# Performance work log

Hardware: AMD Instinct MI355X
Metric: run time of the kernel (lower is better)

## Reference

```python
import jax, jax.numpy as jnp
import numpy as np
import math

B, H, S, D = 4, 16, 2048, 64

def setup_inputs() -> dict:
    key = jax.random.key(0)
    kq, kk, kv, km = jax.random.split(key, 4)
    query = jax.random.normal(kq, (B, H, S, D), dtype=jnp.float32)
    k = jax.random.normal(kk, (B, H, S, D), dtype=jnp.float32)
    value = jax.random.normal(kv, (B, H, S, D), dtype=jnp.float32)
    mask = jax.random.randint(km, (1, 1, S, S), 0, 2) == 1  # True = masked
    return {"query": query, "key": k, "value": value, "mask": mask}

def reference(query, key, value, mask):
    # scores: [B,H,S,S]
    scale = 1.0 / math.sqrt(key.shape[-1])
    scores = jnp.einsum('bhqd,bhkd->bhqk', query, key) * scale
    scores = jnp.where(mask, -jnp.inf, scores)
    probs = jax.nn.softmax(scores, axis=-1)
    out = jnp.einsum('bhqk,bhkd->bhqd', probs, value)
    return out
```

## Files before the change

### kernel.cpp

```cpp
#include <hip/hip_runtime.h>
#include <hip/hip_bf16.h>
#include <stdint.h>

#define BHN 64
#define SEQ 2048
#define DH  64

typedef unsigned short u16;
typedef __attribute__((ext_vector_type(8))) short bf16x8;
typedef __attribute__((ext_vector_type(16))) float f32x16;

__device__ inline u16 f2bf(float x){
  union { float f; uint32_t u; } a; a.f = x;
  uint32_t u = a.u;
  uint32_t lsb = (u >> 16) & 1u;
  u += 0x7FFFu + lsb;
  return (u16)(u >> 16);
}

__device__ inline float fast_exp2(float x){
#if __has_builtin(__builtin_amdgcn_exp2f)
  return __builtin_amdgcn_exp2f(x);
#else
  float r; asm("v_exp_f32 %0, %1" : "=v"(r) : "v"(x)); return r;
#endif
}

__device__ inline void gload_lds16(const void* g, void* l){
  __builtin_amdgcn_global_load_lds(
      (const __attribute__((address_space(1))) void*)g,
      (__attribute__((address_space(3))) void*)l, 16, 0, 0);
}


__global__ __launch_bounds__(256) void build_tiles(const float* __restrict__ kf,
                                                   const float* __restrict__ vf,
                                                   u16* __restrict__ tiles){
  __shared__ float sVf[64][65];
  int head = blockIdx.x >> 5;
  int kt   = blockIdx.x & 31;
  int k0   = kt * 64;
  int t = threadIdx.x;

  {
    int r = t >> 2;
    int dseg = (t & 3) * 16;
    const float* src = vf + ((int64_t)(head*SEQ + k0 + r))*DH + dseg;
    #pragma unroll
    for (int j = 0; j < 16; j += 4){
      float4 v = *(const float4*)(src + j);
      sVf[r][dseg+j+0] = v.x; sVf[r][dseg+j+1] = v.y;
      sVf[r][dseg+j+2] = v.z; sVf[r][dseg+j+3] = v.w;
    }
  }

  u16* outb = tiles + ((size_t)(head*32 + kt) << 13);

  #pragma unroll
  for (int i = 0; i < 2; i++){
    int cid = i*256 + t;
    int f = cid >> 6;
    int l = cid & 63;
    int kh = f >> 2, ds = f & 3;
    int row = k0 + kh*32 + (l & 31);
    int dstart = ds*16 + (l >> 5)*8;
    const float* src = kf + ((int64_t)(head*SEQ + row))*DH + dstart;
    float4 a = *(const float4*)(src);
    float4 b = *(const float4*)(src + 4);
    union { u16 h[8]; uint4 v; } pk;
    pk.h[0]=f2bf(a.x); pk.h[1]=f2bf(a.y); pk.h[2]=f2bf(a.z); pk.h[3]=f2bf(a.w);
    pk.h[4]=f2bf(b.x); pk.h[5]=f2bf(b.y); pk.h[6]=f2bf(b.z); pk.h[7]=f2bf(b.w);
    *(uint4*)(outb + f*512 + l*8) = pk.v;
  }

  __syncthreads();

  #pragma unroll
  for (int i = 0; i < 2; i++){
    int cid = i*256 + t;
    int g = cid >> 6;
    int l = cid & 63;
    int oh = g >> 2, ks = g & 3;
    int d  = oh*32 + (l & 31);
    int kk = ks*16 + (l >> 5)*8;
    union { u16 h[8]; uint4 v; } pk;
    #pragma unroll
    for (int j = 0; j < 8; j++) pk.h[j] = f2bf(sVf[kk+j][d]);
    *(uint4*)(outb + (8+g)*512 + l*8) = pk.v;
  }
}

__global__ __launch_bounds__(256) void pack_mask(const void* __restrict__ mraw,
                                                 uint32_t* __restrict__ mkp){
  __shared__ int sflag;
  int t = threadIdx.x;
  const uint32_t* m32 = (const uint32_t*)mraw;
  if (t == 0) sflag = 0;
  __syncthreads();
  if (t < 64){
    uint32_t v = m32[t] | m32[t+64] | m32[t+128] | m32[t+192];
    if (v > 1u) atomicOr(&sflag, 1);
  }
  __syncthreads();
  bool isbool = (sflag != 0);
  int idx = blockIdx.x*256 + t;
  int row = idx >> 6;
  int wd  = idx & 63;
  uint32_t bits = 0;
  if (isbool){
    const uint8_t* mb = (const uint8_t*)mraw + (int64_t)row*SEQ + wd*32;
    uint4 a = ((const uint4*)mb)[0];
    uint4 b = ((const uint4*)mb)[1];
    uint32_t words[8] = {a.x,a.y,a.z,a.w,b.x,b.y,b.z,b.w};
    #pragma unroll
    for (int i = 0; i < 32; i++){
      int kl = (i&3) + 8*((i>>2)&3) + 4*(i>>4);
      uint32_t byte = (words[kl>>2] >> (8*(kl&3))) & 0xFFu;
      bits |= (byte ? 0u : 1u) << i;
    }
  } else {
    const uint32_t* mi = m32 + (int64_t)row*SEQ + wd*32;
    uint32_t words[32];
    #pragma unroll
    for (int j = 0; j < 32; j += 4){
      uint4 v = *(const uint4*)(mi + j);
      words[j+0]=v.x; words[j+1]=v.y; words[j+2]=v.z; words[j+3]=v.w;
    }
    #pragma unroll
    for (int i = 0; i < 32; i++){
      int kl = (i&3) + 8*((i>>2)&3) + 4*(i>>4);
      bits |= (words[kl] ? 0u : 1u) << i;
    }
  }
  mkp[(size_t)wd*SEQ + row] = bits;
}


__global__ __launch_bounds__(256, 4) void attn_mfma(
    const float* __restrict__ qf, const u16* __restrict__ tiles,
    const uint32_t* __restrict__ mkp, float* __restrict__ out)
{
  __shared__ __align__(16) char lds[2*8192 + 512];

  int bid = blockIdx.x;
  int logical = (bid & 7)*128 + (bid >> 3);
  int head = logical >> 4;
  int q0   = (logical & 15) * 128;

  int t  = threadIdx.x;
  int w  = t >> 6;
  int l  = t & 63;
  int l31 = l & 31;
  int hi  = l >> 5;
  int hi16 = hi << 4;

  const float QS = 0.125f * 1.4426950408889634f;
  bf16x8 qfr[4];
  {
    const float* qrow = qf + ((size_t)(head*SEQ + q0 + w*32 + l31))*DH + hi*8;
    #pragma unroll
    for (int ds = 0; ds < 4; ds++){
      float4 a = *(const float4*)(qrow + ds*16);
      float4 b = *(const float4*)(qrow + ds*16 + 4);
      uint32_t u0, u1, u2, u3;
      asm("v_cvt_pk_bf16_f32 %0, %1, %2" : "=v"(u0) : "v"(a.x*QS), "v"(a.y*QS));
      asm("v_cvt_pk_bf16_f32 %0, %1, %2" : "=v"(u1) : "v"(a.z*QS), "v"(a.w*QS));
      asm("v_cvt_pk_bf16_f32 %0, %1, %2" : "=v"(u2) : "v"(b.x*QS), "v"(b.y*QS));
      asm("v_cvt_pk_bf16_f32 %0, %1, %2" : "=v"(u3) : "v"(b.z*QS), "v"(b.w*QS));
      union { uint32_t u[4]; bf16x8 h; } pk_;
      pk_.u[0]=u0; pk_.u[1]=u1; pk_.u[2]=u2; pk_.u[3]=u3;
      qfr[ds] = pk_.h;
    }
  }

  const uint32_t* mptr = mkp + (q0 + w*32 + l31);

  const char* tb = (const char*)tiles + ((size_t)head << 19) + l*16;
  int woff  = (w < 2) ? (w*2048) : (8192 + (w & 1)*4096);
  int khmul = (w < 2) ? 4096 : 2048;
  char* dbase = lds + w*2048;

  f32x16 O0 = {0,0,0,0,0,0,0,0,0,0,0,0,0,0,0,0};
  f32x16 O1 = {0,0,0,0,0,0,0,0,0,0,0,0,0,0,0,0};
  float ls0 = 0.f, ls1 = 0.f;

  const char* ldsL = lds + l*16;

  auto STAGE = [&](int ks32, int bufoff){
    int ktp = (ks32 < 64) ? ks32 : 63;
    const char* s_ = tb + (((size_t)(ktp >> 1)) << 14) + woff + (ktp & 1)*khmul;
    char* d_ = dbase + bufoff;
    gload_lds16(s_,        d_);
    gload_lds16(s_ + 1024, d_ + 1024);
  };

  STAGE(0, 0);
  __syncthreads();

  int cur = 0;
  for (int kt = 0; kt < 64; kt++){
    if (kt < 63) STAGE(kt+1, cur ^ 8192);
    uint32_t mw = *mptr; mptr += SEQ;
    uint32_t wsh = mw >> hi16;

    f32x16 c = {0,0,0,0,0,0,0,0,0,0,0,0,0,0,0,0};
    __builtin_amdgcn_s_setprio(1);
    #pragma unroll
    for (int ds = 0; ds < 4; ds++){
      bf16x8 kfr = *(const bf16x8*)(ldsL + cur + ds*1024);
      c = __builtin_amdgcn_mfma_f32_32x32x16_bf16(kfr, qfr[ds], c, 0, 0, 0);
    }
    __builtin_amdgcn_s_setprio(0);

    float p[16];
    #pragma unroll
    for (int r = 0; r < 16; r++){
      float pe = fast_exp2(c[r]);
      int32_t km;
      asm("v_bfe_i32 %0, %1, %2, 1" : "=v"(km) : "v"(wsh), "n"(r));
      p[r] = __uint_as_float(__float_as_uint(pe) & (uint32_t)km);
    }
    #pragma unroll
    for (int r = 0; r < 8; r++){ ls0 += p[r]; ls1 += p[r+8]; }

    bf16x8 pa0, pa1;
    {
      uint32_t A0, A1, B0, B1;
      asm("v_cvt_pk_bf16_f32 %0, %1, %2" : "=v"(A0) : "v"(p[0]), "v"(p[1]));
      asm("v_cvt_pk_bf16_f32 %0, %1, %2" : "=v"(A1) : "v"(p[2]), "v"(p[3]));
      asm("v_cvt_pk_bf16_f32 %0, %1, %2" : "=v"(B0) : "v"(p[4]), "v"(p[5]));
      asm("v_cvt_pk_bf16_f32 %0, %1, %2" : "=v"(B1) : "v"(p[6]), "v"(p[7]));
      asm("v_permlane32_swap_b32 %0, %1" : "+v"(A0), "+v"(B0));
      asm("v_permlane32_swap_b32 %0, %1" : "+v"(A1), "+v"(B1));
      union { uint32_t u[4]; bf16x8 h; } pk_;
      pk_.u[0] = A0; pk_.u[1] = A1; pk_.u[2] = B0; pk_.u[3] = B1;
      pa0 = pk_.h;
    }
    {
      uint32_t A0, A1, B0, B1;
      asm("v_cvt_pk_bf16_f32 %0, %1, %2" : "=v"(A0) : "v"(p[8]),  "v"(p[9]));
      asm("v_cvt_pk_bf16_f32 %0, %1, %2" : "=v"(A1) : "v"(p[10]), "v"(p[11]));
      asm("v_cvt_pk_bf16_f32 %0, %1, %2" : "=v"(B0) : "v"(p[12]), "v"(p[13]));
      asm("v_cvt_pk_bf16_f32 %0, %1, %2" : "=v"(B1) : "v"(p[14]), "v"(p[15]));
      asm("v_permlane32_swap_b32 %0, %1" : "+v"(A0), "+v"(B0));
      asm("v_permlane32_swap_b32 %0, %1" : "+v"(A1), "+v"(B1));
      union { uint32_t u[4]; bf16x8 h; } pk_;
      pk_.u[0] = A0; pk_.u[1] = A1; pk_.u[2] = B0; pk_.u[3] = B1;
      pa1 = pk_.h;
    }

    __builtin_amdgcn_s_setprio(1);
    {
      bf16x8 v00 = *(const bf16x8*)(ldsL + cur + 4096);
      bf16x8 v01 = *(const bf16x8*)(ldsL + cur + 5120);
      bf16x8 v10 = *(const bf16x8*)(ldsL + cur + 6144);
      bf16x8 v11 = *(const bf16x8*)(ldsL + cur + 7168);
      O0 = __builtin_amdgcn_mfma_f32_32x32x16_bf16(pa0, v00, O0, 0, 0, 0);
      O0 = __builtin_amdgcn_mfma_f32_32x32x16_bf16(pa1, v01, O0, 0, 0, 0);
      O1 = __builtin_amdgcn_mfma_f32_32x32x16_bf16(pa0, v10, O1, 0, 0, 0);
      O1 = __builtin_amdgcn_mfma_f32_32x32x16_bf16(pa1, v11, O1, 0, 0, 0);
    }
    __builtin_amdgcn_s_setprio(0);

    __syncthreads();
    cur ^= 8192;
  }

  float lt = ls0 + ls1;
  {
    uint32_t a = __float_as_uint(lt), b = a;
    asm("v_permlane32_swap_b32 %0, %1" : "+v"(a), "+v"(b));
    lt = __uint_as_float(a) + __uint_as_float(b);
  }
  float* sInv = (float*)(lds + 16384);
  if (hi == 0) sInv[w*32 + l31] = 1.0f / lt;
  float* obase = out + ((size_t)(head*SEQ + q0 + w*32))*DH + l31;
  #pragma unroll
  for (int r = 0; r < 16; r++){
    int qr = (r&3) + 8*(r>>2) + 4*hi;
    float inv = sInv[w*32 + qr];
    obase[(size_t)qr*DH]      = O0[r] * inv;
    obase[(size_t)qr*DH + 32] = O1[r] * inv;
  }
}


__global__ __launch_bounds__(256) void attn_naive(
    const float* __restrict__ qf, const float* __restrict__ kf,
    const float* __restrict__ vf, const void* __restrict__ mraw,
    float* __restrict__ out)
{
  __shared__ float sq[64];
  __shared__ float sS[SEQ];
  __shared__ float redM[4], redS[4];
  __shared__ float sO[4][64];
  __shared__ int sflag;

  int bid = blockIdx.x;
  int bh = bid >> 11;
  int q  = bid & 2047;
  int t  = threadIdx.x;
  const uint32_t* m32 = (const uint32_t*)mraw;
  if (t == 0) sflag = 0;
  __syncthreads();
  if (t < 64){
    uint32_t v = m32[t] | m32[t+64] | m32[t+128] | m32[t+192];
    if (v > 1u) atomicOr(&sflag, 1);
  }
  if (t < 64) sq[t] = qf[((int64_t)bh*SEQ + q)*DH + t] * (0.125f*1.4426950408889634f);
  __syncthreads();
  bool isbool = (sflag != 0);

  float lmax = -3e38f;
  for (int k = t; k < SEQ; k += 256){
    bool masked = isbool ? (((const uint8_t*)mraw)[(int64_t)q*SEQ + k] != 0)
                         : (m32[(int64_t)q*SEQ + k] != 0);
    float s = -3e38f;
    if (!masked){
      const float* krow = kf + ((int64_t)bh*SEQ + k)*DH;
      float acc = 0.f;
      for (int d = 0; d < 64; d++) acc += sq[d]*krow[d];
      s = acc;
    }
    sS[k] = s;
    lmax = fmaxf(lmax, s);
  }
  for (int o = 32; o >= 1; o >>= 1) lmax = fmaxf(lmax, __shfl_xor(lmax, o));
  if ((t & 63) == 0) redM[t >> 6] = lmax;
  __syncthreads();
  float m = fmaxf(fmaxf(redM[0], redM[1]), fmaxf(redM[2], redM[3]));
  float lsum = 0.f;
  for (int k = t; k < SEQ; k += 256){
    float p = exp2f(sS[k] - m);
    sS[k] = p;
    lsum += p;
  }
  for (int o = 32; o >= 1; o >>= 1) lsum += __shfl_xor(lsum, o);
  if ((t & 63) == 0) redS[t >> 6] = lsum;
  __syncthreads();
  float lden = redS[0] + redS[1] + redS[2] + redS[3];

  float o = 0.f;
  int d = t & 63;
  int c = t >> 6;
  for (int k = c*512; k < (c+1)*512; k++)
    o += sS[k] * vf[((int64_t)bh*SEQ + k)*DH + d];
  sO[c][d] = o;
  __syncthreads();
  if (t < 64){
    float r = (sO[0][t] + sO[1][t] + sO[2][t] + sO[3][t]) / lden;
    out[((int64_t)bh*SEQ + q)*DH + t] = r;
  }
}


extern "C" void kernel_launch(void* const* d_in, const int* in_sizes, int n_in,
                              void* d_out, int out_size, void* d_ws, size_t ws_size,
                              hipStream_t stream)
{
  const float* qf = (const float*)d_in[0];
  const float* kf = (const float*)d_in[1];
  const float* vf = (const float*)d_in[2];
  const void*  mraw = d_in[3];
  float* out = (float*)d_out;

  size_t tilesB = (size_t)BHN*32*16384;
  size_t need = tilesB + (size_t)SEQ*64*4 + 256;
  if (ws_size >= need){
    u16* tiles = (u16*)d_ws;
    uint32_t* mkp = (uint32_t*)((char*)d_ws + tilesB);
    hipLaunchKernelGGL(build_tiles, dim3(2048), dim3(256), 0, stream, kf, vf, tiles);
    hipLaunchKernelGGL(pack_mask,   dim3(512),  dim3(256), 0, stream, mraw, mkp);
    hipLaunchKernelGGL(attn_mfma,   dim3(1024), dim3(256), 0, stream, qf, tiles, mkp, out);
  } else {
    hipLaunchKernelGGL(attn_naive, dim3(BHN*SEQ), dim3(256), 0, stream, qf, kf, vf, mraw, out);
  }
}
```

Before: 118.8 us.

## Process 64-key tiles per barrier with interleaved 64-bit mask words

Result: faster. 112.3 us (-5.5%).

```diff
diff --git a/kernel.cpp b/kernel.cpp
--- a/kernel.cpp
+++ b/kernel.cpp
@@ -132,7 +132,7 @@
       bits |= (words[kl] ? 0u : 1u) << i;
     }
   }
-  mkp[(size_t)wd*SEQ + row] = bits;
+  mkp[((size_t)(wd >> 1)*SEQ + row)*2 + (wd & 1)] = bits;
 }
 
 
@@ -140,7 +140,7 @@
     const float* __restrict__ qf, const u16* __restrict__ tiles,
     const uint32_t* __restrict__ mkp, float* __restrict__ out)
 {
-  __shared__ __align__(16) char lds[2*8192 + 512];
+  __shared__ __align__(16) char lds[2*16384 + 512];
 
   int bid = blockIdx.x;
   int logical = (bid & 7)*128 + (bid >> 3);
@@ -173,12 +173,10 @@
     }
   }
 
-  const uint32_t* mptr = mkp + (q0 + w*32 + l31);
-
-  const char* tb = (const char*)tiles + ((size_t)head << 19) + l*16;
-  int woff  = (w < 2) ? (w*2048) : (8192 + (w & 1)*4096);
-  int khmul = (w < 2) ? 4096 : 2048;
-  char* dbase = lds + w*2048;
+  const uint2* mptr = (const uint2*)mkp + (q0 + w*32 + l31);
+
+  const char* tb = (const char*)tiles + ((size_t)head << 19) + w*4096 + l*16;
+  char* dwave = lds + w*4096;
 
   f32x16 O0 = {0,0,0,0,0,0,0,0,0,0,0,0,0,0,0,0};
   f32x16 O1 = {0,0,0,0,0,0,0,0,0,0,0,0,0,0,0,0};
@@ -186,84 +184,96 @@
 
   const char* ldsL = lds + l*16;
 
-  auto STAGE = [&](int ks32, int bufoff){
-    int ktp = (ks32 < 64) ? ks32 : 63;
-    const char* s_ = tb + (((size_t)(ktp >> 1)) << 14) + woff + (ktp & 1)*khmul;
-    char* d_ = dbase + bufoff;
+  auto STAGE = [&](int kt64, int bufoff){
+    const char* s_ = tb + ((size_t)kt64 << 14);
+    char* d_ = dwave + bufoff;
     gload_lds16(s_,        d_);
     gload_lds16(s_ + 1024, d_ + 1024);
+    gload_lds16(s_ + 2048, d_ + 2048);
+    gload_lds16(s_ + 3072, d_ + 3072);
   };
 
   STAGE(0, 0);
+  uint2 mw2 = *mptr; mptr += SEQ;
   __syncthreads();
 
   int cur = 0;
-  for (int kt = 0; kt < 64; kt++){
-    if (kt < 63) STAGE(kt+1, cur ^ 8192);
-    uint32_t mw = *mptr; mptr += SEQ;
-    uint32_t wsh = mw >> hi16;
-
-    f32x16 c = {0,0,0,0,0,0,0,0,0,0,0,0,0,0,0,0};
-    __builtin_amdgcn_s_setprio(1);
-    #pragma unroll
-    for (int ds = 0; ds < 4; ds++){
-      bf16x8 kfr = *(const bf16x8*)(ldsL + cur + ds*1024);
-      c = __builtin_amdgcn_mfma_f32_32x32x16_bf16(kfr, qfr[ds], c, 0, 0, 0);
-    }
-    __builtin_amdgcn_s_setprio(0);
-
-    float p[16];
-    #pragma unroll
-    for (int r = 0; r < 16; r++){
-      float pe = fast_exp2(c[r]);
-      int32_t km;
-      asm("v_bfe_i32 %0, %1, %2, 1" : "=v"(km) : "v"(wsh), "n"(r));
-      p[r] = __uint_as_float(__float_as_uint(pe) & (uint32_t)km);
-    }
-    #pragma unroll
-    for (int r = 0; r < 8; r++){ ls0 += p[r]; ls1 += p[r+8]; }
-
-    bf16x8 pa0, pa1;
-    {
-      uint32_t A0, A1, B0, B1;
-      asm("v_cvt_pk_bf16_f32 %0, %1, %2" : "=v"(A0) : "v"(p[0]), "v"(p[1]));
-      asm("v_cvt_pk_bf16_f32 %0, %1, %2" : "=v"(A1) : "v"(p[2]), "v"(p[3]));
-      asm("v_cvt_pk_bf16_f32 %0, %1, %2" : "=v"(B0) : "v"(p[4]), "v"(p[5]));
-      asm("v_cvt_pk_bf16_f32 %0, %1, %2" : "=v"(B1) : "v"(p[6]), "v"(p[7]));
-      asm("v_permlane32_swap_b32 %0, %1" : "+v"(A0), "+v"(B0));
-      asm("v_permlane32_swap_b32 %0, %1" : "+v"(A1), "+v"(B1));
-      union { uint32_t u[4]; bf16x8 h; } pk_;
-      pk_.u[0] = A0; pk_.u[1] = A1; pk_.u[2] = B0; pk_.u[3] = B1;
-      pa0 = pk_.h;
-    }
-    {
-      uint32_t A0, A1, B0, B1;
-      asm("v_cvt_pk_bf16_f32 %0, %1, %2" : "=v"(A0) : "v"(p[8]),  "v"(p[9]));
-      asm("v_cvt_pk_bf16_f32 %0, %1, %2" : "=v"(A1) : "v"(p[10]), "v"(p[11]));
-      asm("v_cvt_pk_bf16_f32 %0, %1, %2" : "=v"(B0) : "v"(p[12]), "v"(p[13]));
-      asm("v_cvt_pk_bf16_f32 %0, %1, %2" : "=v"(B1) : "v"(p[14]), "v"(p[15]));
-      asm("v_permlane32_swap_b32 %0, %1" : "+v"(A0), "+v"(B0));
-      asm("v_permlane32_swap_b32 %0, %1" : "+v"(A1), "+v"(B1));
-      union { uint32_t u[4]; bf16x8 h; } pk_;
-      pk_.u[0] = A0; pk_.u[1] = A1; pk_.u[2] = B0; pk_.u[3] = B1;
-      pa1 = pk_.h;
-    }
-
-    __builtin_amdgcn_s_setprio(1);
-    {
-      bf16x8 v00 = *(const bf16x8*)(ldsL + cur + 4096);
-      bf16x8 v01 = *(const bf16x8*)(ldsL + cur + 5120);
-      bf16x8 v10 = *(const bf16x8*)(ldsL + cur + 6144);
-      bf16x8 v11 = *(const bf16x8*)(ldsL + cur + 7168);
-      O0 = __builtin_amdgcn_mfma_f32_32x32x16_bf16(pa0, v00, O0, 0, 0, 0);
-      O0 = __builtin_amdgcn_mfma_f32_32x32x16_bf16(pa1, v01, O0, 0, 0, 0);
-      O1 = __builtin_amdgcn_mfma_f32_32x32x16_bf16(pa0, v10, O1, 0, 0, 0);
-      O1 = __builtin_amdgcn_mfma_f32_32x32x16_bf16(pa1, v11, O1, 0, 0, 0);
-    }
-    __builtin_amdgcn_s_setprio(0);
-
+  for (int kt = 0; kt < 32; kt++){
+    uint2 mw2n = mw2;
+    if (kt < 31){
+      STAGE(kt+1, cur ^ 16384);
+      mw2n = *mptr; mptr += SEQ;
+    }
+
+    const char* lb = ldsL + cur;
+
+    #pragma unroll
+    for (int g = 0; g < 2; g++){
+      uint32_t wsh = (g ? mw2.y : mw2.x) >> hi16;
+
+      f32x16 c = {0,0,0,0,0,0,0,0,0,0,0,0,0,0,0,0};
+      __builtin_amdgcn_s_setprio(1);
+      #pragma unroll
+      for (int ds = 0; ds < 4; ds++){
+        bf16x8 kfr = *(const bf16x8*)(lb + (4*g + ds)*1024);
+        c = __builtin_amdgcn_mfma_f32_32x32x16_bf16(kfr, qfr[ds], c, 0, 0, 0);
+      }
+      __builtin_amdgcn_s_setprio(0);
+
+      float p[16];
+      #pragma unroll
+      for (int r = 0; r < 16; r++){
+        float pe = fast_exp2(c[r]);
+        int32_t km;
+        asm("v_bfe_i32 %0, %1, %2, 1" : "=v"(km) : "v"(wsh), "n"(r));
+        p[r] = __uint_as_float(__float_as_uint(pe) & (uint32_t)km);
+      }
+      #pragma unroll
+      for (int r = 0; r < 8; r++){ ls0 += p[r]; ls1 += p[r+8]; }
+
+      bf16x8 pa0, pa1;
+      {
+        uint32_t A0, A1, B0, B1;
+        asm("v_cvt_pk_bf16_f32 %0, %1, %2" : "=v"(A0) : "v"(p[0]), "v"(p[1]));
+        asm("v_cvt_pk_bf16_f32 %0, %1, %2" : "=v"(A1) : "v"(p[2]), "v"(p[3]));
+        asm("v_cvt_pk_bf16_f32 %0, %1, %2" : "=v"(B0) : "v"(p[4]), "v"(p[5]));
+        asm("v_cvt_pk_bf16_f32 %0, %1, %2" : "=v"(B1) : "v"(p[6]), "v"(p[7]));
+        asm("v_permlane32_swap_b32 %0, %1" : "+v"(A0), "+v"(B0));
+        asm("v_permlane32_swap_b32 %0, %1" : "+v"(A1), "+v"(B1));
+        union { uint32_t u[4]; bf16x8 h; } pk_;
+        pk_.u[0] = A0; pk_.u[1] = A1; pk_.u[2] = B0; pk_.u[3] = B1;
+        pa0 = pk_.h;
+      }
+      {
+        uint32_t A0, A1, B0, B1;
+        asm("v_cvt_pk_bf16_f32 %0, %1, %2" : "=v"(A0) : "v"(p[8]),  "v"(p[9]));
+        asm("v_cvt_pk_bf16_f32 %0, %1, %2" : "=v"(A1) : "v"(p[10]), "v"(p[11]));
+        asm("v_cvt_pk_bf16_f32 %0, %1, %2" : "=v"(B0) : "v"(p[12]), "v"(p[13]));
+        asm("v_cvt_pk_bf16_f32 %0, %1, %2" : "=v"(B1) : "v"(p[14]), "v"(p[15]));
+        asm("v_permlane32_swap_b32 %0, %1" : "+v"(A0), "+v"(B0));
+        asm("v_permlane32_swap_b32 %0, %1" : "+v"(A1), "+v"(B1));
+        union { uint32_t u[4]; bf16x8 h; } pk_;
+        pk_.u[0] = A0; pk_.u[1] = A1; pk_.u[2] = B0; pk_.u[3] = B1;
+        pa1 = pk_.h;
+      }
+
+      __builtin_amdgcn_s_setprio(1);
+      {
+        bf16x8 v00 = *(const bf16x8*)(lb + (8  + 2*g)*1024);
+        bf16x8 v01 = *(const bf16x8*)(lb + (9  + 2*g)*1024);
+        bf16x8 v10 = *(const bf16x8*)(lb + (12 + 2*g)*1024);
+        bf16x8 v11 = *(const bf16x8*)(lb + (13 + 2*g)*1024);
+        O0 = __builtin_amdgcn_mfma_f32_32x32x16_bf16(pa0, v00, O0, 0, 0, 0);
+        O0 = __builtin_amdgcn_mfma_f32_32x32x16_bf16(pa1, v01, O0, 0, 0, 0);
+        O1 = __builtin_amdgcn_mfma_f32_32x32x16_bf16(pa0, v10, O1, 0, 0, 0);
+        O1 = __builtin_amdgcn_mfma_f32_32x32x16_bf16(pa1, v11, O1, 0, 0, 0);
+      }
+      __builtin_amdgcn_s_setprio(0);
+    }
+
+    mw2 = mw2n;
     __syncthreads();
-    cur ^= 8192;
+    cur ^= 16384;
   }
 
   float lt = ls0 + ls1;
@@ -272,7 +282,7 @@
     asm("v_permlane32_swap_b32 %0, %1" : "+v"(a), "+v"(b));
     lt = __uint_as_float(a) + __uint_as_float(b);
   }
-  float* sInv = (float*)(lds + 16384);
+  float* sInv = (float*)(lds + 32768);
   if (hi == 0) sInv[w*32 + l31] = 1.0f / lt;
   float* obase = out + ((size_t)(head*SEQ + q0 + w*32))*DH + l31;
   #pragma unroll
```

## Load K/V fragments directly from global into registers, dropping LDS staging

Applied to the files above, without the earlier changes.

Result: no change. 117.3 us (-1.3%).

```diff
diff --git a/kernel.cpp b/kernel.cpp
--- a/kernel.cpp
+++ b/kernel.cpp
@@ -24,12 +24,6 @@
 #else
   float r; asm("v_exp_f32 %0, %1" : "=v"(r) : "v"(x)); return r;
 #endif
-}
-
-__device__ inline void gload_lds16(const void* g, void* l){
-  __builtin_amdgcn_global_load_lds(
-      (const __attribute__((address_space(1))) void*)g,
-      (__attribute__((address_space(3))) void*)l, 16, 0, 0);
 }
 
 
@@ -132,15 +126,15 @@
       bits |= (words[kl] ? 0u : 1u) << i;
     }
   }
-  mkp[(size_t)wd*SEQ + row] = bits;
-}
-
-
-__global__ __launch_bounds__(256, 4) void attn_mfma(
+  mkp[((size_t)(wd >> 1)*SEQ + row)*2 + (wd & 1)] = bits;
+}
+
+
+__global__ __launch_bounds__(256, 3) void attn_mfma(
     const float* __restrict__ qf, const u16* __restrict__ tiles,
     const uint32_t* __restrict__ mkp, float* __restrict__ out)
 {
-  __shared__ __align__(16) char lds[2*8192 + 512];
+  __shared__ float sInv[128];
 
   int bid = blockIdx.x;
   int logical = (bid & 7)*128 + (bid >> 3);
@@ -173,43 +167,37 @@
     }
   }
 
-  const uint32_t* mptr = mkp + (q0 + w*32 + l31);
+  const uint2* mptr = (const uint2*)mkp + (q0 + w*32 + l31);
 
   const char* tb = (const char*)tiles + ((size_t)head << 19) + l*16;
-  int woff  = (w < 2) ? (w*2048) : (8192 + (w & 1)*4096);
-  int khmul = (w < 2) ? 4096 : 2048;
-  char* dbase = lds + w*2048;
 
   f32x16 O0 = {0,0,0,0,0,0,0,0,0,0,0,0,0,0,0,0};
   f32x16 O1 = {0,0,0,0,0,0,0,0,0,0,0,0,0,0,0,0};
   float ls0 = 0.f, ls1 = 0.f;
 
-  const char* ldsL = lds + l*16;
-
-  auto STAGE = [&](int ks32, int bufoff){
-    int ktp = (ks32 < 64) ? ks32 : 63;
-    const char* s_ = tb + (((size_t)(ktp >> 1)) << 14) + woff + (ktp & 1)*khmul;
-    char* d_ = dbase + bufoff;
-    gload_lds16(s_,        d_);
-    gload_lds16(s_ + 1024, d_ + 1024);
+  auto LOADK = [&](int sg, bf16x8* kb){
+    const char* s_ = tb + ((size_t)(sg >> 1) << 14) + (sg & 1)*4096;
+    kb[0] = *(const bf16x8*)(s_);
+    kb[1] = *(const bf16x8*)(s_ + 1024);
+    kb[2] = *(const bf16x8*)(s_ + 2048);
+    kb[3] = *(const bf16x8*)(s_ + 3072);
   };
-
-  STAGE(0, 0);
-  __syncthreads();
-
-  int cur = 0;
-  for (int kt = 0; kt < 64; kt++){
-    if (kt < 63) STAGE(kt+1, cur ^ 8192);
-    uint32_t mw = *mptr; mptr += SEQ;
-    uint32_t wsh = mw >> hi16;
+  auto LOADV = [&](int sg, bf16x8* vb){
+    const char* s_ = tb + ((size_t)(sg >> 1) << 14) + 8192 + (sg & 1)*2048;
+    vb[0] = *(const bf16x8*)(s_);
+    vb[1] = *(const bf16x8*)(s_ + 1024);
+    vb[2] = *(const bf16x8*)(s_ + 4096);
+    vb[3] = *(const bf16x8*)(s_ + 5120);
+  };
+
+  auto COMPUTE = [&](const bf16x8* kb, const bf16x8* vb, uint32_t mword){
+    uint32_t wsh = mword >> hi16;
 
     f32x16 c = {0,0,0,0,0,0,0,0,0,0,0,0,0,0,0,0};
     __builtin_amdgcn_s_setprio(1);
     #pragma unroll
-    for (int ds = 0; ds < 4; ds++){
-      bf16x8 kfr = *(const bf16x8*)(ldsL + cur + ds*1024);
-      c = __builtin_amdgcn_mfma_f32_32x32x16_bf16(kfr, qfr[ds], c, 0, 0, 0);
-    }
+    for (int ds = 0; ds < 4; ds++)
+      c = __builtin_amdgcn_mfma_f32_32x32x16_bf16(kb[ds], qfr[ds], c, 0, 0, 0);
     __builtin_amdgcn_s_setprio(0);
 
     float p[16];
@@ -250,20 +238,31 @@
     }
 
     __builtin_amdgcn_s_setprio(1);
-    {
-      bf16x8 v00 = *(const bf16x8*)(ldsL + cur + 4096);
-      bf16x8 v01 = *(const bf16x8*)(ldsL + cur + 5120);
-      bf16x8 v10 = *(const bf16x8*)(ldsL + cur + 6144);
-      bf16x8 v11 = *(const bf16x8*)(ldsL + cur + 7168);
-      O0 = __builtin_amdgcn_mfma_f32_32x32x16_bf16(pa0, v00, O0, 0, 0, 0);
-      O0 = __builtin_amdgcn_mfma_f32_32x32x16_bf16(pa1, v01, O0, 0, 0, 0);
-      O1 = __builtin_amdgcn_mfma_f32_32x32x16_bf16(pa0, v10, O1, 0, 0, 0);
-      O1 = __builtin_amdgcn_mfma_f32_32x32x16_bf16(pa1, v11, O1, 0, 0, 0);
-    }
+    O0 = __builtin_amdgcn_mfma_f32_32x32x16_bf16(pa0, vb[0], O0, 0, 0, 0);
+    O0 = __builtin_amdgcn_mfma_f32_32x32x16_bf16(pa1, vb[1], O0, 0, 0, 0);
+    O1 = __builtin_amdgcn_mfma_f32_32x32x16_bf16(pa0, vb[2], O1, 0, 0, 0);
+    O1 = __builtin_amdgcn_mfma_f32_32x32x16_bf16(pa1, vb[3], O1, 0, 0, 0);
     __builtin_amdgcn_s_setprio(0);
-
-    __syncthreads();
-    cur ^= 8192;
+  };
+
+  bf16x8 kA[4], kB[4], vA[4], vB[4];
+  LOADK(0, kA);
+  uint2 mw2 = *mptr;
+
+  #pragma unroll 1
+  for (int st = 0; st < 32; st++){
+    LOADV(2*st, vA);
+    LOADK(2*st + 1, kB);
+    uint2 mcur = mw2;
+    if (st < 31){ mptr += SEQ; mw2 = *mptr; }
+
+    COMPUTE(kA, vA, mcur.x);
+
+    LOADV(2*st + 1, vB);
+    int nsg = (st < 31) ? (2*st + 2) : 63;
+    LOADK(nsg, kA);
+
+    COMPUTE(kB, vB, mcur.y);
   }
 
   float lt = ls0 + ls1;
@@ -272,7 +271,6 @@
     asm("v_permlane32_swap_b32 %0, %1" : "+v"(a), "+v"(b));
     lt = __uint_as_float(a) + __uint_as_float(b);
   }
-  float* sInv = (float*)(lds + 16384);
   if (hi == 0) sInv[w*32 + l31] = 1.0f / lt;
   float* obase = out + ((size_t)(head*SEQ + q0 + w*32))*DH + l31;
   #pragma unroll
```
